# Optimization experiments

Measured on AMD Instinct MI355X. Metric: run time of the kernel, lower is better.

The kernel has to match this reference:

```python
import jax, jax.numpy as jnp
import numpy as np

EMBED_DIM = 768
NUM_PATCHES = 196
PATCH = 16
NUM_HEADS = 12
HEAD_DIM = 64
NUM_LAYERS = 1
NUM_TIME_STEPS = 6
HOP_HID = 3072
ALPHA = 1.0
BETA = 1.0 / np.sqrt(HEAD_DIM)
EPS = 1e-5
PATCH_DIM = PATCH * PATCH * 3


def layernorm(x, gamma, beta):
    mu = jnp.mean(x, axis=-1, keepdims=True)
    var = jnp.var(x, axis=-1, keepdims=True)
    return gamma * (x - mu) / jnp.sqrt(var + EPS) + beta


def patchify(x):
    # x: [B, C, H, W] -> [B, N, C*P*P]
    B, C, H, W = x.shape
    hp, wp = H // PATCH, W // PATCH
    x = x.reshape(B, C, hp, PATCH, wp, PATCH)
    x = x.transpose(0, 2, 4, 1, 3, 5)  # [B, hp, wp, C, P, P]
    return x.reshape(B, hp * wp, C * PATCH * PATCH)


def block_energy(g, wq, wk, xi):
    # Energy attention: no value matrix; E = -1/beta * sum_{h, queries} logsumexp_keys(beta * K.Q)
    q = jnp.einsum('bnd,hdk->bhnk', g, wq)
    k = jnp.einsum('bnd,hdk->bhnk', g, wk)
    a = jnp.einsum('bhnk,bhmk->bhnm', k, q)  # [B,H,keys,queries]
    e_attn = -(1.0 / BETA) * jnp.sum(jax.nn.logsumexp(BETA * a, axis=2))
    # Hopfield energy
    h = jax.nn.relu(g @ xi)  # [B,N,HOP_HID]
    e_hop = -0.5 * jnp.sum(h * h)
    return e_attn + e_hop


def setup_inputs() -> dict:
    key = jax.random.key(0)
    ks = jax.random.split(key, 12)
    s = 0.02
    return {
        'x': jax.random.normal(ks[0], (16, 3, 224, 224), dtype=jnp.float32),
        'patch_w': jax.random.normal(ks[1], (PATCH_DIM, EMBED_DIM), dtype=jnp.float32) * s,
        'patch_b': jnp.zeros((EMBED_DIM,), dtype=jnp.float32),
        'cls_token': jnp.ones((1, 1, EMBED_DIM), dtype=jnp.float32),
        'pos_embed': jax.random.normal(ks[2], (1, NUM_PATCHES + 1, EMBED_DIM), dtype=jnp.float32) * 0.002,
        'ln_gamma': jnp.ones((EMBED_DIM,), dtype=jnp.float32),
        'ln_beta': jnp.zeros((EMBED_DIM,), dtype=jnp.float32),
        'wq': jax.random.normal(ks[3], (NUM_HEADS, EMBED_DIM, HEAD_DIM), dtype=jnp.float32) * s,
        'wk': jax.random.normal(ks[4], (NUM_HEADS, EMBED_DIM, HEAD_DIM), dtype=jnp.float32) * s,
        'xi': jax.random.normal(ks[5], (EMBED_DIM, HOP_HID), dtype=jnp.float32) * s,
        'out_gamma': jnp.ones((EMBED_DIM,), dtype=jnp.float32),
        'out_beta': jnp.zeros((EMBED_DIM,), dtype=jnp.float32),
        'out_w': jax.random.normal(ks[6], (EMBED_DIM, PATCH_DIM), dtype=jnp.float32) * s,
        'out_b': jnp.zeros((PATCH_DIM,), dtype=jnp.float32),
    }


def reference(x, patch_w, patch_b, cls_token, pos_embed, ln_gamma, ln_beta,
              wq, wk, xi, out_gamma, out_beta, out_w, out_b):
    B = x.shape[0]
    tok = patchify(x) @ patch_w + patch_b                 # [B, N, D]
    cls = jnp.broadcast_to(cls_token, (B, 1, EMBED_DIM))
    h = jnp.concatenate([cls, tok], axis=1) + pos_embed   # [B, N+1, D]

    grad_fn = jax.grad(lambda g: block_energy(g, wq, wk, xi))
    for _layer in range(NUM_LAYERS):
        for _t in range(NUM_TIME_STEPS):
            g = layernorm(h, ln_gamma, ln_beta)
            h = h - ALPHA * grad_fn(g)

    out = layernorm(h, out_gamma, out_beta) @ out_w + out_b
    return out[:, 1:]  # reconstructed patches [B, N, PATCH_DIM]
```

## Files before the change

kernel.cpp:

```cpp
#include <hip/hip_runtime.h>

#define NB 16
#define NTOK 197
#define NPATCH 196
#define D 768
#define NH 12
#define HD 64
#define HOP 3072
#define TSTEPS 6
#define BETA_F 0.125f
#define PLD 208
#define PBH (NTOK * PLD)
#define NROWS (NB * NTOK)
#define NPROWS (NB * NPATCH)
#define AROWS 3200
#define DD (768 * 768)
#define DH (768 * 3072)
#define SZL ((long)NROWS * D)

typedef unsigned short u16;
typedef __attribute__((ext_vector_type(8))) _Float16 f16x8;
typedef __attribute__((ext_vector_type(4))) float f32x4;

#define FLAG_ACC 1
#define FLAG_RELU 2
#define FLAG_H16 4

__device__ __forceinline__ u16 f2h(float f) {
    union { _Float16 h; u16 u; } cv;
    cv.h = (_Float16)f;
    return cv.u;
}
__device__ __forceinline__ float h2f(u16 v) {
    union { _Float16 h; u16 u; } cv;
    cv.u = v;
    return (float)cv.h;
}

__device__ __forceinline__ void gld16(const void* g, void* l) {
    __builtin_amdgcn_global_load_lds((const __attribute__((address_space(1))) void*)g,
                                     (__attribute__((address_space(3))) void*)l, 16, 0, 0);
}

__device__ __forceinline__ int xcd_swz900(int bid) {
    int xcd = bid & 7, k = bid >> 3;
    return (xcd < 4 ? xcd * 113 : 452 + (xcd - 4) * 112) + k;
}

__global__ __launch_bounds__(256) void gemm_h16(
    const u16* __restrict__ A, const u16* __restrict__ B,
    void* __restrict__ Cv, const float* __restrict__ bias,
    int M, int N, int K, int lda, int ldbt, int ldc, int flags,
    long sAz, long sBz, long sCz) {
    __shared__ __align__(16) u16 As[128 * 32];
    __shared__ __align__(16) u16 Bs[128 * 32];
    int zz = blockIdx.z;
    A += (long)zz * sAz;
    B += (long)zz * sBz;
    long czoff = (long)zz * sCz;
    int t = threadIdx.x;
    int w = t >> 6, lane = t & 63;
    int lr = lane & 15, lg = lane >> 4;
    int wr = w >> 1, wc = w & 1;
    long row0 = (long)blockIdx.y * 128, col0 = (long)blockIdx.x * 128;

    f32x4 acc[4][4];
#pragma unroll
    for (int i = 0; i < 4; i++)
#pragma unroll
        for (int j = 0; j < 4; j++) acc[i][j] = (f32x4){0.f, 0.f, 0.f, 0.f};

    int c0 = w * 64 + lane;
    int r0s = c0 >> 2, k0s = (((c0 & 3) ^ ((r0s >> 1) & 3)) << 3);
    int c1 = 256 + w * 64 + lane;
    int r1s = c1 >> 2, k1s = (((c1 & 3) ^ ((r1s >> 1) & 3)) << 3);

    for (int kt = 0; kt < K; kt += 32) {
        const u16* AB = A + row0 * lda + kt;
        const u16* BB = B + col0 * ldbt + kt;
        gld16(AB + (long)r0s * lda + k0s, (char*)As + (w * 64) * 16);
        gld16(AB + (long)r1s * lda + k1s, (char*)As + (256 + w * 64) * 16);
        gld16(BB + (long)r0s * ldbt + k0s, (char*)Bs + (w * 64) * 16);
        gld16(BB + (long)r1s * ldbt + k1s, (char*)Bs + (256 + w * 64) * 16);
        __syncthreads();
        f16x8 af[4], bf[4];
#pragma unroll
        for (int mi = 0; mi < 4; mi++) {
            int row = wr * 64 + mi * 16 + lr;
            af[mi] = *(const f16x8*)&As[row * 32 + ((lg ^ ((row >> 1) & 3)) << 3)];
        }
#pragma unroll
        for (int ni = 0; ni < 4; ni++) {
            int row = wc * 64 + ni * 16 + lr;
            bf[ni] = *(const f16x8*)&Bs[row * 32 + ((lg ^ ((row >> 1) & 3)) << 3)];
        }
#pragma unroll
        for (int mi = 0; mi < 4; mi++)
#pragma unroll
            for (int ni = 0; ni < 4; ni++)
                acc[mi][ni] = __builtin_amdgcn_mfma_f32_16x16x32_f16(af[mi], bf[ni], acc[mi][ni], 0, 0, 0);
        __syncthreads();
    }

    long mbase = row0 + wr * 64;
    long nbase = col0 + wc * 64;
#pragma unroll
    for (int mi = 0; mi < 4; mi++) {
#pragma unroll
        for (int r = 0; r < 4; r++) {
            long grow = mbase + mi * 16 + lg * 4 + r;
            if (grow >= M) continue;
#pragma unroll
            for (int ni = 0; ni < 4; ni++) {
                long gcol = nbase + ni * 16 + lr;
                float v = acc[mi][ni][r];
                if (bias) v += bias[gcol];
                if (flags & FLAG_RELU) v = fmaxf(v, 0.f);
                long idx = czoff + grow * ldc + gcol;
                if (flags & FLAG_ACC) ((float*)Cv)[idx] += v;
                else if (flags & FLAG_H16) ((u16*)Cv)[idx] = f2h(v);
                else ((float*)Cv)[idx] = v;
            }
        }
    }
}

__global__ __launch_bounds__(256) void fused_proj(
    const u16* __restrict__ A,
    const u16* __restrict__ WQT, const u16* __restrict__ WKT, const u16* __restrict__ XIT,
    u16* __restrict__ Qh, u16* __restrict__ Kh, u16* __restrict__ HH) {
    __shared__ __align__(16) u16 As[128 * 32];
    __shared__ __align__(16) u16 Bs[128 * 32];
    int lid = xcd_swz900(blockIdx.x);
    int cx = lid % 36, by = lid / 36;
    const u16* B; int ldc; long col0; int mode;
    if (cx < 6)       { B = WQT; ldc = 768;  col0 = (long)cx * 128;        mode = 0; }
    else if (cx < 12) { B = WKT; ldc = 768;  col0 = (long)(cx - 6) * 128;  mode = 1; }
    else              { B = XIT; ldc = 3072; col0 = (long)(cx - 12) * 128; mode = 2; }
    int t = threadIdx.x;
    int w = t >> 6, lane = t & 63;
    int lr = lane & 15, lg = lane >> 4;
    int wr = w >> 1, wc = w & 1;
    long row0 = (long)by * 128;

    f32x4 acc[4][4];
#pragma unroll
    for (int i = 0; i < 4; i++)
#pragma unroll
        for (int j = 0; j < 4; j++) acc[i][j] = (f32x4){0.f, 0.f, 0.f, 0.f};

    int c0 = w * 64 + lane;
    int r0s = c0 >> 2, k0s = (((c0 & 3) ^ ((r0s >> 1) & 3)) << 3);
    int c1 = 256 + w * 64 + lane;
    int r1s = c1 >> 2, k1s = (((c1 & 3) ^ ((r1s >> 1) & 3)) << 3);

    for (int kt = 0; kt < 768; kt += 32) {
        const u16* AB = A + row0 * 768 + kt;
        const u16* BB = B + col0 * 768 + kt;
        gld16(AB + (long)r0s * 768 + k0s, (char*)As + (w * 64) * 16);
        gld16(AB + (long)r1s * 768 + k1s, (char*)As + (256 + w * 64) * 16);
        gld16(BB + (long)r0s * 768 + k0s, (char*)Bs + (w * 64) * 16);
        gld16(BB + (long)r1s * 768 + k1s, (char*)Bs + (256 + w * 64) * 16);
        __syncthreads();
        f16x8 af[4], bf[4];
#pragma unroll
        for (int mi = 0; mi < 4; mi++) {
            int row = wr * 64 + mi * 16 + lr;
            af[mi] = *(const f16x8*)&As[row * 32 + ((lg ^ ((row >> 1) & 3)) << 3)];
        }
#pragma unroll
        for (int ni = 0; ni < 4; ni++) {
            int row = wc * 64 + ni * 16 + lr;
            bf[ni] = *(const f16x8*)&Bs[row * 32 + ((lg ^ ((row >> 1) & 3)) << 3)];
        }
#pragma unroll
        for (int mi = 0; mi < 4; mi++)
#pragma unroll
            for (int ni = 0; ni < 4; ni++)
                acc[mi][ni] = __builtin_amdgcn_mfma_f32_16x16x32_f16(af[mi], bf[ni], acc[mi][ni], 0, 0, 0);
        __syncthreads();
    }

    long mbase = row0 + wr * 64;
    long nbase = col0 + wc * 64;
#pragma unroll
    for (int mi = 0; mi < 4; mi++) {
#pragma unroll
        for (int r = 0; r < 4; r++) {
            long grow = mbase + mi * 16 + lg * 4 + r;
            if (grow >= NROWS) continue;
#pragma unroll
            for (int ni = 0; ni < 4; ni++) {
                long gcol = nbase + ni * 16 + lr;
                float v = acc[mi][ni][r];
                long idx = grow * ldc + gcol;
                if (mode == 0)      Qh[idx] = f2h(v);
                else if (mode == 1) Kh[idx] = f2h(v);
                else                HH[idx] = f2h(fmaxf(v, 0.f));
            }
        }
    }
}

__global__ __launch_bounds__(256) void gemm_h16_fused(
    const u16* __restrict__ G1, const u16* __restrict__ G2, const u16* __restrict__ HH,
    const u16* __restrict__ WQ, const u16* __restrict__ WK, const u16* __restrict__ XB,
    u16* __restrict__ part) {
    __shared__ __align__(16) u16 As[128 * 32];
    __shared__ __align__(16) u16 Bs[128 * 32];
    int lid = xcd_swz900(blockIdx.x);
    int bx = lid % 6, by = (lid / 6) % 25, zz = lid / 150;
    const u16* A; const u16* B; int lda; int K0;
    if (zz == 0)      { A = G1; B = WQ; lda = 768;  K0 = 0; }
    else if (zz == 1) { A = G2; B = WK; lda = 768;  K0 = 0; }
    else              { A = HH; B = XB; lda = 3072; K0 = (zz - 2) * 768; }
    u16* C = part + (long)zz * SZL;

    int t = threadIdx.x;
    int w = t >> 6, lane = t & 63;
    int lr = lane & 15, lg = lane >> 4;
    int wr = w >> 1, wc = w & 1;
    long row0 = (long)by * 128, col0 = (long)bx * 128;

    f32x4 acc[4][4];
#pragma unroll
    for (int i = 0; i < 4; i++)
#pragma unroll
        for (int j = 0; j < 4; j++) acc[i][j] = (f32x4){0.f, 0.f, 0.f, 0.f};

    int c0 = w * 64 + lane;
    int r0s = c0 >> 2, k0s = (((c0 & 3) ^ ((r0s >> 1) & 3)) << 3);
    int c1 = 256 + w * 64 + lane;
    int r1s = c1 >> 2, k1s = (((c1 & 3) ^ ((r1s >> 1) & 3)) << 3);

    for (int kt = K0; kt < K0 + 768; kt += 32) {
        const u16* AB = A + row0 * lda + kt;
        const u16* BB = B + col0 * (long)lda + kt;
        gld16(AB + (long)r0s * lda + k0s, (char*)As + (w * 64) * 16);
        gld16(AB + (long)r1s * lda + k1s, (char*)As + (256 + w * 64) * 16);
        gld16(BB + (long)r0s * lda + k0s, (char*)Bs + (w * 64) * 16);
        gld16(BB + (long)r1s * lda + k1s, (char*)Bs + (256 + w * 64) * 16);
        __syncthreads();
        f16x8 af[4], bf[4];
#pragma unroll
        for (int mi = 0; mi < 4; mi++) {
            int row = wr * 64 + mi * 16 + lr;
            af[mi] = *(const f16x8*)&As[row * 32 + ((lg ^ ((row >> 1) & 3)) << 3)];
        }
#pragma unroll
        for (int ni = 0; ni < 4; ni++) {
            int row = wc * 64 + ni * 16 + lr;
            bf[ni] = *(const f16x8*)&Bs[row * 32 + ((lg ^ ((row >> 1) & 3)) << 3)];
        }
#pragma unroll
        for (int mi = 0; mi < 4; mi++)
#pragma unroll
            for (int ni = 0; ni < 4; ni++)
                acc[mi][ni] = __builtin_amdgcn_mfma_f32_16x16x32_f16(af[mi], bf[ni], acc[mi][ni], 0, 0, 0);
        __syncthreads();
    }

    long mbase = row0 + wr * 64;
    long nbase = col0 + wc * 64;
#pragma unroll
    for (int mi = 0; mi < 4; mi++) {
#pragma unroll
        for (int r = 0; r < 4; r++) {
            long grow = mbase + mi * 16 + lg * 4 + r;
            if (grow >= NROWS) continue;
#pragma unroll
            for (int ni = 0; ni < 4; ni++) {
                long gcol = nbase + ni * 16 + lr;
                C[grow * D + gcol] = f2h(acc[mi][ni][r]);
            }
        }
    }
}

__global__ __launch_bounds__(256) void ln_fuse_kernel(
    float* __restrict__ X, u16* __restrict__ Yh16, const u16* __restrict__ part,
    const float* __restrict__ gamma, const float* __restrict__ beta,
    int compact, int doReduce, int writeBack) {
    int r = blockIdx.x;
    long xrow = compact ? ((long)(r / NPATCH) * NTOK + 1 + (r % NPATCH)) : (long)r;
    float* x = X + xrow * D;
    int t = threadIdx.x;
    float v[3];
    float s = 0.f, ss = 0.f;
#pragma unroll
    for (int i = 0; i < 3; i++) {
        int c = t + 256 * i;
        float val = x[c];
        if (doReduce) {
            long off = xrow * D + c;
            float p01 = h2f(part[off]) + h2f(part[SZL + off]);
            float p23 = h2f(part[2 * SZL + off]) + h2f(part[3 * SZL + off]);
            float p45 = h2f(part[4 * SZL + off]) + h2f(part[5 * SZL + off]);
            val += (p01 + p23) + p45;
            if (writeBack) x[c] = val;
        }
        v[i] = val;
        s += val;
        ss += val * val;
    }
    __shared__ float red[8];
    for (int off = 32; off; off >>= 1) {
        s += __shfl_down(s, off, 64);
        ss += __shfl_down(ss, off, 64);
    }
    int wid = t >> 6, lane = t & 63;
    if (lane == 0) { red[wid] = s; red[4 + wid] = ss; }
    __syncthreads();
    s = red[0] + red[1] + red[2] + red[3];
    ss = red[4] + red[5] + red[6] + red[7];
    float mu = s * (1.f / 768.f);
    float var = ss * (1.f / 768.f) - mu * mu;
    float inv = rsqrtf(var + 1e-5f);
#pragma unroll
    for (int i = 0; i < 3; i++) {
        int c = t + 256 * i;
        float yv = gamma[c] * (v[i] - mu) * inv + beta[c];
        Yh16[(long)r * D + c] = f2h(yv);
    }
}

__global__ __launch_bounds__(256) void attn_p_kernel(const u16* __restrict__ Q, const u16* __restrict__ K,
                                                     u16* __restrict__ Pt) {
    __shared__ __align__(16) u16 Ks[NTOK][72];
    int bh = blockIdx.x, mt = blockIdx.y;
    int b = bh / NH, h = bh % NH;
    int t = threadIdx.x;
    const u16* Kb = K + (long)b * NTOK * D + h * HD;
    for (int i = t; i < NTOK * 8; i += 256) {
        int n = i >> 3, c8 = (i & 7) << 3;
        *(uint4*)&Ks[n][c8] = *(const uint4*)(Kb + (long)n * D + c8);
    }
    __syncthreads();
    int ql = t >> 4, l16 = t & 15;
    int m = mt * 16 + ql;
    int mr = m < NTOK ? m : NTOK - 1;
    const u16* Qrow = Q + (long)(b * NTOK + mr) * D + h * HD;
    float q[64];
#pragma unroll
    for (int k = 0; k < 64; k += 8) {
        f16x8 v = *(const f16x8*)(Qrow + k);
#pragma unroll
        for (int j = 0; j < 8; j++) q[k + j] = (float)v[j];
    }
    float s[13];
    float mx = -1e30f;
#pragma unroll
    for (int i = 0; i < 13; i++) {
        int n = i * 16 + l16;
        const u16* kr = Ks[n < NTOK ? n : 0];
        float a0 = 0.f, a1 = 0.f, a2 = 0.f, a3 = 0.f;
#pragma unroll
        for (int k = 0; k < 64; k += 8) {
            f16x8 kv = *(const f16x8*)&kr[k];
            a0 += (float)kv[0] * q[k]     + (float)kv[4] * q[k + 4];
            a1 += (float)kv[1] * q[k + 1] + (float)kv[5] * q[k + 5];
            a2 += (float)kv[2] * q[k + 2] + (float)kv[6] * q[k + 6];
            a3 += (float)kv[3] * q[k + 3] + (float)kv[7] * q[k + 7];
        }
        float sv = ((a0 + a1) + (a2 + a3)) * BETA_F;
        s[i] = (n < NTOK) ? sv : -1e30f;
        mx = fmaxf(mx, s[i]);
    }
    mx = fmaxf(mx, __shfl_xor(mx, 1, 64));
    mx = fmaxf(mx, __shfl_xor(mx, 2, 64));
    mx = fmaxf(mx, __shfl_xor(mx, 4, 64));
    mx = fmaxf(mx, __shfl_xor(mx, 8, 64));
    float ssum = 0.f;
#pragma unroll
    for (int i = 0; i < 13; i++) {
        float e = (s[i] > -1e29f) ? __expf(s[i] - mx) : 0.f;
        s[i] = e;
        ssum += e;
    }
    ssum += __shfl_xor(ssum, 1, 64);
    ssum += __shfl_xor(ssum, 2, 64);
    ssum += __shfl_xor(ssum, 4, 64);
    ssum += __shfl_xor(ssum, 8, 64);
    float inv = 1.f / ssum;
    if (m < NTOK) {
        u16* PtB = Pt + (long)bh * PBH;
#pragma unroll
        for (int i = 0; i < 13; i++) {
            int n = i * 16 + l16;
            PtB[(long)m * PLD + n] = (n < NTOK) ? f2h(s[i] * inv) : (u16)0;
        }
    }
}

__global__ __launch_bounds__(256) void attn_g_kernel(
    const u16* __restrict__ Pt, const u16* __restrict__ Qh, const u16* __restrict__ Kh,
    u16* __restrict__ G1, u16* __restrict__ G2) {
    __shared__ float As[16][68];
    __shared__ float Bs[16][68];
    int z = blockIdx.z;
    int which = z / 192, bh = z - which * 192;
    int b = bh / NH, h = bh % NH;
    const u16* A = Pt + (long)bh * PBH;
    const u16* B = (which ? Qh : Kh) + (long)b * NTOK * D + h * HD;
    u16* G = which ? G2 : G1;

    int t = threadIdx.x;
    int tx = t & 15, ty = t >> 4;
    int row0 = blockIdx.y * 64;

    float acc[4][4] = {};

    for (int kt = 0; kt < NTOK; kt += 16) {
        if (which == 0) {
            int r = t >> 2, c4 = (t & 3) << 2;
            int gr = row0 + r, gk = kt + c4;
            float4 v = make_float4(0.f, 0.f, 0.f, 0.f);
            if (gr < NTOK) {
                ushort4 u = *(const ushort4*)(A + (long)gr * PLD + gk);
                v = make_float4(h2f(u.x), h2f(u.y), h2f(u.z), h2f(u.w));
            }
            As[c4 + 0][r] = v.x; As[c4 + 1][r] = v.y; As[c4 + 2][r] = v.z; As[c4 + 3][r] = v.w;
        } else {
            int rr = t >> 4, c4 = (t & 15) << 2;
            int gk = kt + rr, gc = row0 + c4;
            float4 v = make_float4(0.f, 0.f, 0.f, 0.f);
            if (gk < NTOK && gc + 3 < PLD) {
                ushort4 u = *(const ushort4*)(A + (long)gk * PLD + gc);
                v = make_float4(h2f(u.x), h2f(u.y), h2f(u.z), h2f(u.w));
            }
            As[rr][c4 + 0] = v.x; As[rr][c4 + 1] = v.y; As[rr][c4 + 2] = v.z; As[rr][c4 + 3] = v.w;
        }
        {
            int r = t >> 4, c4 = (t & 15) << 2;
            int gk = kt + r;
            float4 v = make_float4(0.f, 0.f, 0.f, 0.f);
            if (gk < NTOK) {
                ushort4 u = *(const ushort4*)(B + (long)gk * D + c4);
                v = make_float4(h2f(u.x), h2f(u.y), h2f(u.z), h2f(u.w));
            }
            Bs[r][c4 + 0] = v.x; Bs[r][c4 + 1] = v.y; Bs[r][c4 + 2] = v.z; Bs[r][c4 + 3] = v.w;
        }
        __syncthreads();
#pragma unroll
        for (int kk = 0; kk < 16; kk++) {
            float av[4], bv[4];
#pragma unroll
            for (int i = 0; i < 4; i++) av[i] = As[kk][ty * 4 + i];
#pragma unroll
            for (int j = 0; j < 4; j++) bv[j] = Bs[kk][tx * 4 + j];
#pragma unroll
            for (int i = 0; i < 4; i++)
#pragma unroll
                for (int j = 0; j < 4; j++) acc[i][j] += av[i] * bv[j];
        }
        __syncthreads();
    }
#pragma unroll
    for (int i = 0; i < 4; i++) {
        int gr = row0 + ty * 4 + i;
        if (gr >= NTOK) continue;
#pragma unroll
        for (int j = 0; j < 4; j++) {
            int gc = tx * 4 + j;
            long idx = ((long)(b * NTOK + gr)) * D + h * HD + gc;
            G[idx] = f2h(acc[i][j]);
        }
    }
}


__global__ __launch_bounds__(256) void patchify_kernel(const float* __restrict__ x, u16* __restrict__ tok) {
    int idx = blockIdx.x * 256 + threadIdx.x;
    const int total = NB * NPATCH * D;
    if (idx >= total) return;
    int d = idx % D;
    int p = (idx / D) % NPATCH;
    int b = idx / (D * NPATCH);
    int c = d >> 8;
    int pi = (d >> 4) & 15;
    int pj = d & 15;
    int hp = p / 14, wp = p % 14;
    int row = hp * 16 + pi, col = wp * 16 + pj;
    tok[idx] = f2h(x[(((long)b * 3 + c) * 224 + row) * 224 + col]);
}

__global__ __launch_bounds__(256) void cls_pos_kernel(float* __restrict__ h, const float* __restrict__ cls,
                                                      const float* __restrict__ pos) {
    int idx = blockIdx.x * 256 + threadIdx.x;
    const int total = NB * NTOK * D;
    if (idx >= total) return;
    int d = idx % D;
    int n = (idx / D) % NTOK;
    float v = pos[n * D + d];
    if (n == 0) h[idx] = cls[d] + v;
    else        h[idx] = h[idx] + v;
}

__global__ __launch_bounds__(256) void wcat_kernel(const float* __restrict__ w, float* __restrict__ Wm) {
    int idx = blockIdx.x * 256 + threadIdx.x;
    const int total = NH * D * HD;
    if (idx >= total) return;
    int k = idx & 63;
    int d = (idx >> 6) % D;
    int hh = idx / (D * HD);
    Wm[d * D + hh * HD + k] = w[idx];
}

__global__ __launch_bounds__(256) void prep_transpose_h(const float* __restrict__ src,
                                                        u16* __restrict__ dst, int R, int C) {
    __shared__ float tile[32][33];
    int c0 = blockIdx.x * 32, r0 = blockIdx.y * 32;
    int tx = threadIdx.x & 31, ty = threadIdx.x >> 5;
    for (int i = ty; i < 32; i += 8)
        tile[i][tx] = src[(long)(r0 + i) * C + c0 + tx];
    __syncthreads();
    for (int i = ty; i < 32; i += 8)
        dst[(long)(c0 + i) * R + r0 + tx] = f2h(tile[tx][i]);
}
__global__ __launch_bounds__(256) void prep_convert_h(const float* __restrict__ src,
                                                      u16* __restrict__ dst, int n) {
    int idx = blockIdx.x * 256 + threadIdx.x;
    if (idx >= n) return;
    dst[idx] = f2h(src[idx]);
}

extern "C" void kernel_launch(void* const* d_in, const int* in_sizes, int n_in,
                              void* d_out, int out_size, void* d_ws, size_t ws_size,
                              hipStream_t stream) {
    const float* x        = (const float*)d_in[0];
    const float* patch_w  = (const float*)d_in[1];
    const float* patch_b  = (const float*)d_in[2];
    const float* cls_tok  = (const float*)d_in[3];
    const float* pos_emb  = (const float*)d_in[4];
    const float* ln_gamma = (const float*)d_in[5];
    const float* ln_beta  = (const float*)d_in[6];
    const float* wq       = (const float*)d_in[7];
    const float* wk       = (const float*)d_in[8];
    const float* xi       = (const float*)d_in[9];
    const float* out_gamma= (const float*)d_in[10];
    const float* out_beta = (const float*)d_in[11];
    const float* out_w    = (const float*)d_in[12];
    const float* out_b    = (const float*)d_in[13];
    float* out = (float*)d_out;

    float* ws = (float*)d_ws;
    const long SZ = SZL;
    const long AR = (long)AROWS * D;
    float* h  = ws;
    u16* gh16    = (u16*)(ws + SZ);
    u16* Qh16    = gh16 + AR;
    u16* Kh16    = Qh16 + AR;
    u16* WmQTh16 = Kh16 + AR;
    u16* WmKTh16 = WmQTh16 + DD;
    u16* WmQh16  = WmKTh16 + DD;
    u16* WmKh16  = WmQh16 + DD;
    u16* xiTh16  = WmKh16 + DD;
    u16* xibh16  = xiTh16 + DH;
    u16* G1h16   = xibh16 + DH;
    u16* G2h16   = G1h16 + AR;
    u16* HH16    = G2h16 + AR;
    u16* owTh16  = HH16 + (long)AROWS * HOP;
    u16* pwTh16  = owTh16 + DD;
    char* R1c = (char*)(pwTh16 + DD);
    u16* Pt16   = (u16*)R1c;
    u16* part16 = (u16*)R1c;
    u16* tok16  = (u16*)R1c;
    float* WmQ  = (float*)(R1c + (size_t)6 * SZ * 2);
    float* WmK  = WmQ + DD;

    patchify_kernel<<<(NB * NPATCH * D + 255) / 256, 256, 0, stream>>>(x, tok16);
    wcat_kernel<<<(NH * D * HD + 255) / 256, 256, 0, stream>>>(wq, WmQ);
    wcat_kernel<<<(NH * D * HD + 255) / 256, 256, 0, stream>>>(wk, WmK);
    prep_transpose_h<<<dim3(24, 24), 256, 0, stream>>>(WmQ, WmQTh16, 768, 768);
    prep_transpose_h<<<dim3(24, 24), 256, 0, stream>>>(WmK, WmKTh16, 768, 768);
    prep_convert_h<<<(DD + 255) / 256, 256, 0, stream>>>(WmQ, WmQh16, DD);
    prep_convert_h<<<(DD + 255) / 256, 256, 0, stream>>>(WmK, WmKh16, DD);
    prep_transpose_h<<<dim3(96, 24), 256, 0, stream>>>(xi, xiTh16, 768, HOP);
    prep_convert_h<<<(DH + 255) / 256, 256, 0, stream>>>(xi, xibh16, DH);
    prep_transpose_h<<<dim3(24, 24), 256, 0, stream>>>(out_w, owTh16, 768, 768);
    prep_transpose_h<<<dim3(24, 24), 256, 0, stream>>>(patch_w, pwTh16, 768, 768);
    gemm_h16<<<dim3(6, 2, NB), 256, 0, stream>>>(
        tok16, pwTh16, h + D, patch_b,
        NPATCH, D, D, D, D, D, 0,
        (long)NPATCH * D, 0, (long)NTOK * D);
    cls_pos_kernel<<<(NB * NTOK * D + 255) / 256, 256, 0, stream>>>(h, cls_tok, pos_emb);

    for (int step = 0; step < TSTEPS; step++) {
        ln_fuse_kernel<<<NROWS, 256, 0, stream>>>(h, gh16, part16, ln_gamma, ln_beta,
                                                  0, step > 0 ? 1 : 0, 1);
        fused_proj<<<900, 256, 0, stream>>>(gh16, WmQTh16, WmKTh16, xiTh16, Qh16, Kh16, HH16);
        attn_p_kernel<<<dim3(192, 13), 256, 0, stream>>>(Qh16, Kh16, Pt16);
        attn_g_kernel<<<dim3(1, 4, 384), 256, 0, stream>>>(Pt16, Qh16, Kh16, G1h16, G2h16);
        gemm_h16_fused<<<900, 256, 0, stream>>>(
            G1h16, G2h16, HH16, WmQh16, WmKh16, xibh16, part16);
    }

    ln_fuse_kernel<<<NPROWS, 256, 0, stream>>>(h, gh16, part16, out_gamma, out_beta, 1, 1, 0);
    gemm_h16<<<dim3(6, 25, 1), 256, 0, stream>>>(
        gh16, owTh16, out, out_b, NPROWS, D, D, D, D, D, 0, 0, 0, 0);
}
```

Before: 1.151 ms.

## Rewrite attention gradient GEMM with fp16 MFMA and padded probability rows

Replaces the scalar fp32 shared-memory GEMM that computes P·Q and Pᵀ·K per head with a kernel that loads the whole K-extent into LDS as fp16 and uses 16x16x32 f16 MFMA instructions. The probability buffer is padded to 208 rows, with the softmax kernel zeroing padded rows, so tiles need no bounds checks in the reduction dimension. This removes fp32 conversion and scalar FMA cost, but reads a few padded rows past each batch's Q/K and relies on the buffer being large enough.

```diff
diff --git a/kernel.cpp b/kernel.cpp
--- a/kernel.cpp
+++ b/kernel.cpp
@@ -10,7 +10,8 @@
 #define TSTEPS 6
 #define BETA_F 0.125f
 #define PLD 208
-#define PBH (NTOK * PLD)
+#define PROWS 208
+#define PBH (PROWS * PLD)
 #define NROWS (NB * NTOK)
 #define NPROWS (NB * NPATCH)
 #define AROWS 3200
@@ -382,88 +383,96 @@
     ssum += __shfl_xor(ssum, 4, 64);
     ssum += __shfl_xor(ssum, 8, 64);
     float inv = 1.f / ssum;
+    u16* PtB = Pt + (long)bh * PBH;
     if (m < NTOK) {
-        u16* PtB = Pt + (long)bh * PBH;
 #pragma unroll
         for (int i = 0; i < 13; i++) {
             int n = i * 16 + l16;
             PtB[(long)m * PLD + n] = (n < NTOK) ? f2h(s[i] * inv) : (u16)0;
         }
-    }
-}
-
-__global__ __launch_bounds__(256) void attn_g_kernel(
+    } else {
+#pragma unroll
+        for (int i = 0; i < 13; i++) {
+            int n = i * 16 + l16;
+            PtB[(long)m * PLD + n] = 0;
+        }
+    }
+}
+
+__global__ __launch_bounds__(256) void attn_g_mfma(
     const u16* __restrict__ Pt, const u16* __restrict__ Qh, const u16* __restrict__ Kh,
     u16* __restrict__ G1, u16* __restrict__ G2) {
-    __shared__ float As[16][68];
-    __shared__ float Bs[16][68];
+    __shared__ __align__(16) u16 Asm[64][224];
+    __shared__ __align__(16) u16 Bsm[64][224];
     int z = blockIdx.z;
     int which = z / 192, bh = z - which * 192;
     int b = bh / NH, h = bh % NH;
-    const u16* A = Pt + (long)bh * PBH;
-    const u16* B = (which ? Qh : Kh) + (long)b * NTOK * D + h * HD;
+    int row0 = blockIdx.x * 64;
+    const u16* P = Pt + (long)bh * PBH;
+    const u16* B = (which ? Qh : Kh) + ((long)b * NTOK) * D + h * HD;
     u16* G = which ? G2 : G1;
-
     int t = threadIdx.x;
-    int tx = t & 15, ty = t >> 4;
-    int row0 = blockIdx.y * 64;
-
-    float acc[4][4] = {};
-
-    for (int kt = 0; kt < NTOK; kt += 16) {
-        if (which == 0) {
-            int r = t >> 2, c4 = (t & 3) << 2;
-            int gr = row0 + r, gk = kt + c4;
-            float4 v = make_float4(0.f, 0.f, 0.f, 0.f);
-            if (gr < NTOK) {
-                ushort4 u = *(const ushort4*)(A + (long)gr * PLD + gk);
-                v = make_float4(h2f(u.x), h2f(u.y), h2f(u.z), h2f(u.w));
+
+    if (which == 0) {
+        for (int idx = t; idx < 64 * 28; idx += 256) {
+            int r = idx / 28, c8 = (idx % 28) * 8;
+            uint4 v = make_uint4(0, 0, 0, 0);
+            if (row0 + r < PROWS && c8 < PLD)
+                v = *(const uint4*)(P + (long)(row0 + r) * PLD + c8);
+            *(uint4*)&Asm[r][c8] = v;
+        }
+    } else {
+        for (int idx = t; idx < 224 * 8; idx += 256) {
+            int m = idx / 8, j8 = (idx % 8) * 8;
+            u16 vals[8];
+            if (m < PROWS && row0 + j8 < PLD) {
+                *(uint4*)vals = *(const uint4*)(P + (long)m * PLD + row0 + j8);
+            } else {
+#pragma unroll
+                for (int j = 0; j < 8; j++) vals[j] = 0;
             }
-            As[c4 + 0][r] = v.x; As[c4 + 1][r] = v.y; As[c4 + 2][r] = v.z; As[c4 + 3][r] = v.w;
+#pragma unroll
+            for (int j = 0; j < 8; j++) Asm[j8 + j][m] = vals[j];
+        }
+    }
+    for (int idx = t; idx < 224 * 8; idx += 256) {
+        int n = idx / 8, c8 = (idx % 8) * 8;
+        u16 vals[8];
+        if (n < PROWS) {
+            *(uint4*)vals = *(const uint4*)(B + (long)n * D + c8);
         } else {
-            int rr = t >> 4, c4 = (t & 15) << 2;
-            int gk = kt + rr, gc = row0 + c4;
-            float4 v = make_float4(0.f, 0.f, 0.f, 0.f);
-            if (gk < NTOK && gc + 3 < PLD) {
-                ushort4 u = *(const ushort4*)(A + (long)gk * PLD + gc);
-                v = make_float4(h2f(u.x), h2f(u.y), h2f(u.z), h2f(u.w));
+#pragma unroll
+            for (int j = 0; j < 8; j++) vals[j] = 0;
+        }
+#pragma unroll
+        for (int j = 0; j < 8; j++) Bsm[c8 + j][n] = vals[j];
+    }
+    __syncthreads();
+
+    int w = t >> 6, lane = t & 63;
+    int lr = lane & 15, lg = lane >> 4;
+    f32x4 acc[4];
+#pragma unroll
+    for (int i = 0; i < 4; i++) acc[i] = (f32x4){0.f, 0.f, 0.f, 0.f};
+#pragma unroll
+    for (int kt = 0; kt < 224; kt += 32) {
+        f16x8 a = *(const f16x8*)&Asm[w * 16 + lr][kt + lg * 8];
+#pragma unroll
+        for (int ni = 0; ni < 4; ni++) {
+            f16x8 bfr = *(const f16x8*)&Bsm[ni * 16 + lr][kt + lg * 8];
+            acc[ni] = __builtin_amdgcn_mfma_f32_16x16x32_f16(a, bfr, acc[ni], 0, 0, 0);
+        }
+    }
+
+#pragma unroll
+    for (int ni = 0; ni < 4; ni++) {
+#pragma unroll
+        for (int r = 0; r < 4; r++) {
+            int m = row0 + w * 16 + lg * 4 + r;
+            if (m < NTOK) {
+                int c = ni * 16 + lr;
+                G[((long)(b * NTOK + m)) * D + h * HD + c] = f2h(acc[ni][r]);
             }
-            As[rr][c4 + 0] = v.x; As[rr][c4 + 1] = v.y; As[rr][c4 + 2] = v.z; As[rr][c4 + 3] = v.w;
-        }
-        {
-            int r = t >> 4, c4 = (t & 15) << 2;
-            int gk = kt + r;
-            float4 v = make_float4(0.f, 0.f, 0.f, 0.f);
-            if (gk < NTOK) {
-                ushort4 u = *(const ushort4*)(B + (long)gk * D + c4);
-                v = make_float4(h2f(u.x), h2f(u.y), h2f(u.z), h2f(u.w));
-            }
-            Bs[r][c4 + 0] = v.x; Bs[r][c4 + 1] = v.y; Bs[r][c4 + 2] = v.z; Bs[r][c4 + 3] = v.w;
-        }
-        __syncthreads();
-#pragma unroll
-        for (int kk = 0; kk < 16; kk++) {
-            float av[4], bv[4];
-#pragma unroll
-            for (int i = 0; i < 4; i++) av[i] = As[kk][ty * 4 + i];
-#pragma unroll
-            for (int j = 0; j < 4; j++) bv[j] = Bs[kk][tx * 4 + j];
-#pragma unroll
-            for (int i = 0; i < 4; i++)
-#pragma unroll
-                for (int j = 0; j < 4; j++) acc[i][j] += av[i] * bv[j];
-        }
-        __syncthreads();
-    }
-#pragma unroll
-    for (int i = 0; i < 4; i++) {
-        int gr = row0 + ty * 4 + i;
-        if (gr >= NTOK) continue;
-#pragma unroll
-        for (int j = 0; j < 4; j++) {
-            int gc = tx * 4 + j;
-            long idx = ((long)(b * NTOK + gr)) * D + h * HD + gc;
-            G[idx] = f2h(acc[i][j]);
         }
     }
 }
@@ -590,7 +599,7 @@
                                                   0, step > 0 ? 1 : 0, 1);
         fused_proj<<<900, 256, 0, stream>>>(gh16, WmQTh16, WmKTh16, xiTh16, Qh16, Kh16, HH16);
         attn_p_kernel<<<dim3(192, 13), 256, 0, stream>>>(Qh16, Kh16, Pt16);
-        attn_g_kernel<<<dim3(1, 4, 384), 256, 0, stream>>>(Pt16, Qh16, Kh16, G1h16, G2h16);
+        attn_g_mfma<<<dim3(4, 1, 384), 256, 0, stream>>>(Pt16, Qh16, Kh16, G1h16, G2h16);
         gemm_h16_fused<<<900, 256, 0, stream>>>(
             G1h16, G2h16, HH16, WmQh16, WmKh16, xibh16, part16);
     }
```

Result: faster. 1.077 ms (-6.4%).
